# Kernel tuning notes

Measured on AMD Instinct MI355X. Metric: run time of the kernel, lower is better.

The kernel has to match this reference:

```python
import jax, jax.numpy as jnp
import numpy as np
import math

B, N, CS, CZ = 1, 512, 384, 128
GD = 16            # ipa_conf.c_hidden -> num 3D groups G
CH = GD * 3        # per-head hidden = 48
H = 8
PQ, PV = 8, 12
NF = 4             # num_frequencies
INF, EPS = 1e5, 1e-8
CZ4 = CZ // 4


def base_frequencies(num_freqs=NF, base=8.0, max_freq=1.0):
    fs = [min(base ** (-2 * i / num_freqs) * max_freq, max_freq) for i in range(num_freqs)]
    return jnp.asarray(fs, dtype=jnp.float32)


def hat(v):
    # v: [..., 3] -> skew-symmetric [..., 3, 3]
    x, y, z = v[..., 0], v[..., 1], v[..., 2]
    o = jnp.zeros_like(x)
    return jnp.stack([
        jnp.stack([o, -z, y], -1),
        jnp.stack([z, o, -x], -1),
        jnp.stack([-y, x, o], -1)], -2)


def setup_inputs() -> dict:
    key = jax.random.key(0)
    ks = jax.random.split(key, 24)
    std = 0.02
    hc = CH * H
    hpkv = H * (PQ + PV) * 3
    inp = {
        's': jax.random.normal(ks[0], (B, N, CS), jnp.float32),
        'z': jax.random.normal(ks[1], (B, N, N, CZ), jnp.float32),
        'rotvec': jax.random.normal(ks[2], (B, N, 3), jnp.float32),
        'mask': jnp.ones((B, N), jnp.float32),
        'wq': jax.random.normal(ks[3], (CS, hc), jnp.float32) * std,
        'bq': jnp.zeros((hc,), jnp.float32),
        'wkv': jax.random.normal(ks[4], (CS, 2 * hc), jnp.float32) * std,
        'bkv': jnp.zeros((2 * hc,), jnp.float32),
        'wkvp': jax.random.normal(ks[5], (CS, hpkv), jnp.float32) * std,
        'bkvp': jnp.zeros((hpkv,), jnp.float32),
        'wb': jax.random.normal(ks[6], (CZ, H), jnp.float32) * std,
        'bb': jnp.zeros((H,), jnp.float32),
        'wdz': jax.random.normal(ks[7], (CZ, CZ4), jnp.float32) * std,
        'bdz': jnp.zeros((CZ4,), jnp.float32),
        'wout': jax.random.normal(ks[8], (H * (CZ4 + CH + PV * 4), CS), jnp.float32) * std,
        'bout': jnp.zeros((CS,), jnp.float32),
        'log_freq_adj': jax.random.normal(ks[9], (NF,), jnp.float32) * std,
        'group_weights': jax.random.normal(ks[10], (GD,), jnp.float32) * std,
        'freq_weights': jnp.full((NF,), 1.0 / NF, jnp.float32),
    }
    return inp


def reference(s, z, rotvec, mask, wq, bq, wkv, bkv, wkvp, bkvp, wb, bb,
              wdz, bdz, wout, bout, log_freq_adj, group_weights, freq_weights):
    G = GD
    # projections
    q = (s @ wq + bq).reshape(B, N, H, CH)
    kv = (s @ wkv + bkv).reshape(B, N, H, 2 * CH)
    k, v = kv[..., :CH], kv[..., CH:]
    P = PQ + PV
    kvp = (s @ wkvp + bkvp).reshape(B, N, 3, H * P)      # torch split(...,3)+stack(-1)
    kvp = jnp.moveaxis(kvp, -2, -1).reshape(B, N, H, P, 3)
    v_pts = kvp[..., PQ:, :]                             # [B,N,H,PV,3]
    bias = z @ wb + bb                                   # [B,N,N,H]
    # RoPE-inspired multi-frequency Rodrigues rotations
    nrm = jnp.linalg.norm(rotvec, axis=-1, keepdims=True)
    angle = nrm + 1e-8                                   # [B,N,1]
    axis = rotvec / jnp.maximum(nrm, 1e-12)
    freqs = base_frequencies() * jnp.exp(log_freq_adj)   # [F]
    theta = angle * freqs                                # [B,N,F]
    K = hat(axis)                                        # [B,N,3,3]
    K2 = K @ K
    sin_t = jnp.sin(theta)[..., None, None]              # [B,N,F,1,1]
    cos_t = jnp.cos(theta)[..., None, None]
    I3 = jnp.eye(3, dtype=s.dtype)
    R = I3 + sin_t * K[:, :, None] + (1.0 - cos_t) * K2[:, :, None]  # [B,N,F,3,3]
    qg = q.reshape(B, N, H, G, 3)
    kg = k.reshape(B, N, H, G, 3)
    q_rot = jnp.einsum('bnfij,bnhgj->bnhgfi', R, qg)     # [B,N,H,G,F,3]
    k_rot = jnp.einsum('bnfij,bnhgj->bnhgfi', R, kg)
    # aggregation weights (sum over groups, softmax-weighted freqs)
    freq_w = jax.nn.softmax(freq_weights)
    group_w = jax.nn.softplus(group_weights) * math.sqrt(1.0 / G)
    qw = q_rot * freq_w[None, None, None, None, :, None] * group_w[None, None, None, :, None, None]
    scores = jnp.einsum('bihgfc,bjhgfc->bhij', qw, k_rot) / math.sqrt(3.0)
    a = scores + math.sqrt(1.0 / 3.0) * jnp.transpose(bias, (0, 3, 1, 2))
    sq_mask = INF * (mask[:, :, None] * mask[:, None, :] - 1.0)
    a = jax.nn.softmax(a + sq_mask[:, None], axis=-1)    # [B,H,N,N]
    # outputs
    o = jnp.einsum('bhij,bjhc->bihc', a, v).reshape(B, N, H * CH)
    o_pt = jnp.einsum('bhij,bjhpc->bihpc', a, v_pts)     # [B,N,H,PV,3]
    o_pt_norm = jnp.sqrt(jnp.sum(o_pt ** 2, -1) + EPS).reshape(B, N, H * PV)
    o_pt_flat = o_pt.reshape(B, N, H * PV, 3)
    pair_z = z @ wdz + bdz                               # [B,N,N,CZ4]
    o_pair = jnp.einsum('bhij,bijc->bihc', a, pair_z).reshape(B, N, H * CZ4)
    feats = jnp.concatenate([o, o_pt_flat[..., 0], o_pt_flat[..., 1],
                             o_pt_flat[..., 2], o_pt_norm, o_pair], axis=-1)
    return feats @ wout + bout                           # [B,N,CS]
```

## Files before the change

### kernel.cpp

```cpp
#include <hip/hip_runtime.h>
#include <math.h>


#define OFF_PROJ 0
#define SZ_PROJ (512*1632)
#define OFF_QW (OFF_PROJ + SZ_PROJ)
#define SZ_QW (8*512*192)
#define OFF_KST (OFF_QW + SZ_QW)
#define OFF_V (OFF_KST + SZ_QW)
#define SZ_V (512*384)
#define OFF_VP (OFF_V + SZ_V)
#define SZ_VP (512*288)
#define OFF_A (OFF_VP + SZ_VP)
#define SZ_A (8*512*512)
#define OFF_PZ (OFF_A + SZ_A)
#define SZ_PZ (512*512*32)
#define OFF_FEATS (OFF_PZ + SZ_PZ)
#define SZ_FEATS (512*1024)

__global__ __launch_bounds__(256) void proj_kernel(
    const float* __restrict__ s, const float* __restrict__ wq, const float* __restrict__ bq,
    const float* __restrict__ wkv, const float* __restrict__ bkv,
    const float* __restrict__ wkvp, const float* __restrict__ bkvp,
    float* __restrict__ proj)
{
  __shared__ float sA[64][20];
  __shared__ float sB[16][68];
  int ct = blockIdx.x;
  int i0 = blockIdx.y * 64;
  int col0 = ct * 64;
  const float* W; const float* bias; int wld, wcol0;
  if (col0 < 384)       { W = wq;   bias = bq;   wld = 384; wcol0 = col0; }
  else if (col0 < 1152) { W = wkv;  bias = bkv;  wld = 768; wcol0 = col0 - 384; }
  else                  { W = wkvp; bias = bkvp; wld = 480; wcol0 = col0 - 1152; }
  int t = threadIdx.x;
  int tr4 = (t >> 4) * 4;
  int tc4 = (t & 15) * 4;
  float acc[4][4];
  #pragma unroll
  for (int q = 0; q < 4; q++)
    #pragma unroll
    for (int p = 0; p < 4; p++) acc[q][p] = 0.f;
  bool wfull = (wcol0 + 64 <= wld);
  for (int kt = 0; kt < 384; kt += 16){
    {
      int r = t >> 2, k0 = (t & 3) * 4;
      float4 v = *(const float4*)(s + (i0 + r)*384 + kt + k0);
      *(float4*)&sA[r][k0] = v;
    }
    {
      int r = t >> 4, c0 = (t & 15) * 4;
      if (wfull){
        float4 v = *(const float4*)(W + (kt + r)*wld + wcol0 + c0);
        *(float4*)&sB[r][c0] = v;
      } else {
        #pragma unroll
        for (int u = 0; u < 4; u++){
          int wc = wcol0 + c0 + u; if (wc >= wld) wc = wld - 1;
          sB[r][c0+u] = W[(kt + r)*wld + wc];
        }
      }
    }
    __syncthreads();
    #pragma unroll
    for (int k = 0; k < 16; k++){
      float4 bv = *(const float4*)&sB[k][tc4];
      float av[4];
      #pragma unroll
      for (int q = 0; q < 4; q++) av[q] = sA[tr4+q][k];
      #pragma unroll
      for (int q = 0; q < 4; q++){
        acc[q][0] = fmaf(av[q], bv.x, acc[q][0]);
        acc[q][1] = fmaf(av[q], bv.y, acc[q][1]);
        acc[q][2] = fmaf(av[q], bv.z, acc[q][2]);
        acc[q][3] = fmaf(av[q], bv.w, acc[q][3]);
      }
    }
    __syncthreads();
  }
  #pragma unroll
  for (int q = 0; q < 4; q++){
    int row = i0 + tr4 + q;
    #pragma unroll
    for (int p = 0; p < 4; p++){
      int col = col0 + tc4 + p;
      if (col < 1632){
        proj[row*1632 + col] = acc[q][p] + bias[wcol0 + tc4 + p];
      }
    }
  }
}

__global__ __launch_bounds__(128) void node_kernel(
    const float* __restrict__ proj, const float* __restrict__ rotvec,
    const float* __restrict__ lfa, const float* __restrict__ gwts, const float* __restrict__ fwts,
    float* __restrict__ Qw, float* __restrict__ Kst, float* __restrict__ V, float* __restrict__ VP)
{
  int i = blockIdx.x, t = threadIdx.x;
  const float* pr = proj + i*1632;
  float rx = rotvec[i*3], ry = rotvec[i*3+1], rz = rotvec[i*3+2];
  float nrm = sqrtf(rx*rx + ry*ry + rz*rz);
  float angle = nrm + 1e-8f;
  float inv = 1.0f / fmaxf(nrm, 1e-12f);
  float ax = rx*inv, ay = ry*inv, az = rz*inv;
  float f0 = fwts[0], f1 = fwts[1], f2 = fwts[2], f3 = fwts[3];
  float mfw = fmaxf(fmaxf(f0,f1), fmaxf(f2,f3));
  float e0 = expf(f0-mfw), e1 = expf(f1-mfw), e2 = expf(f2-mfw), e3 = expf(f3-mfw);
  float esum = e0+e1+e2+e3;
  float fw[4] = {e0/esum, e1/esum, e2/esum, e3/esum};
  float fq[4] = { 1.0f*expf(lfa[0]), 0.35355339059327373f*expf(lfa[1]),
                  0.125f*expf(lfa[2]), 0.04419417382415922f*expf(lfa[3]) };
  int h = t >> 4, g = t & 15;
  float gw = log1pf(expf(gwts[g])) * 0.25f;
  float q0 = pr[h*48 + g*3 + 0], q1 = pr[h*48 + g*3 + 1], q2 = pr[h*48 + g*3 + 2];
  float k0 = pr[384 + h*96 + g*3 + 0], k1 = pr[384 + h*96 + g*3 + 1], k2 = pr[384 + h*96 + g*3 + 2];
  #pragma unroll
  for (int f = 0; f < 4; f++){
    float th = angle * fq[f];
    float sn = sinf(th), cs = cosf(th), omc = 1.0f - cs;
    float r00 = cs + omc*ax*ax,       r01 = omc*ax*ay - sn*az,  r02 = omc*ax*az + sn*ay;
    float r10 = omc*ay*ax + sn*az,    r11 = cs + omc*ay*ay,     r12 = omc*ay*az - sn*ax;
    float r20 = omc*az*ax - sn*ay,    r21 = omc*az*ay + sn*ax,  r22 = cs + omc*az*az;
    float qr0 = r00*q0 + r01*q1 + r02*q2;
    float qr1 = r10*q0 + r11*q1 + r12*q2;
    float qr2 = r20*q0 + r21*q1 + r22*q2;
    float kr0 = r00*k0 + r01*k1 + r02*k2;
    float kr1 = r10*k0 + r11*k1 + r12*k2;
    float kr2 = r20*k0 + r21*k1 + r22*k2;
    float sc = fw[f] * gw * 0.57735026918962576f;
    int base = (h*512 + i)*192 + (g*4 + f)*3;
    Qw[base+0] = qr0*sc; Qw[base+1] = qr1*sc; Qw[base+2] = qr2*sc;
    Kst[base+0] = kr0;   Kst[base+1] = kr1;   Kst[base+2] = kr2;
  }
  for (int c = t; c < 384; c += 128){
    int hh = c / 48, cc = c % 48;
    V[i*384 + c] = pr[384 + hh*96 + 48 + cc];
  }
  for (int qx = t; qx < 288; qx += 128){
    int ch = qx / 3, c3 = qx % 3;
    int hh = ch / 12, p = ch % 12;
    VP[i*288 + qx] = pr[1152 + c3*160 + hh*20 + 8 + p];
  }
}

__global__ __launch_bounds__(256) void zproj_kernel(
    const float* __restrict__ z, const float* __restrict__ wb, const float* __restrict__ bb,
    const float* __restrict__ wdz, const float* __restrict__ bdz,
    float* __restrict__ biasS, float* __restrict__ PZ)
{
  __shared__ float zs[256][33];
  __shared__ float Wl[40][128];
  int i = blockIdx.y;
  int jt = blockIdx.x;
  int t = threadIdx.x;
  int cg = t >> 6, jg = t & 63;
  for (int e = t; e < 40*128; e += 256){
    int c = e >> 7, k = e & 127;
    Wl[c][k] = (c < 8) ? wb[k*8 + c] : wdz[k*32 + (c - 8)];
  }
  float acc[10][4];
  #pragma unroll
  for (int cc = 0; cc < 10; cc++)
    #pragma unroll
    for (int q = 0; q < 4; q++) acc[cc][q] = 0.f;
  for (int kt = 0; kt < 4; kt++){
    __syncthreads();
    #pragma unroll
    for (int r = 0; r < 8; r++){
      int idx = t + 256*r;
      int jr = idx >> 3, k4 = idx & 7;
      float4 v = *(const float4*)(z + (size_t)(i*512 + jt*256 + jr)*128 + kt*32 + k4*4);
      zs[jr][k4*4+0] = v.x; zs[jr][k4*4+1] = v.y; zs[jr][k4*4+2] = v.z; zs[jr][k4*4+3] = v.w;
    }
    __syncthreads();
    #pragma unroll 4
    for (int k = 0; k < 32; k++){
      float zv[4];
      #pragma unroll
      for (int q = 0; q < 4; q++) zv[q] = zs[q*64 + jg][k];
      #pragma unroll
      for (int cc = 0; cc < 10; cc++){
        float wv = Wl[cg*10 + cc][kt*32 + k];
        #pragma unroll
        for (int q = 0; q < 4; q++) acc[cc][q] = fmaf(zv[q], wv, acc[cc][q]);
      }
    }
  }
  __syncthreads();
  #pragma unroll
  for (int cc = 0; cc < 10; cc++){
    int ch = cg*10 + cc;
    if (ch < 8){
      float bv = bb[ch];
      #pragma unroll
      for (int q = 0; q < 4; q++){
        int j = jt*256 + q*64 + jg;
        biasS[(size_t)ch*262144 + i*512 + j] = 0.57735026918962576f * (acc[cc][q] + bv);
      }
    } else {
      int c = ch - 8;
      float bv = bdz[c];
      #pragma unroll
      for (int q = 0; q < 4; q++){
        zs[q*64 + jg][c] = acc[cc][q] + bv;
      }
    }
  }
  __syncthreads();
  #pragma unroll
  for (int r = 0; r < 8; r++){
    int idx = t + 256*r;
    int jr = idx >> 3, c4 = idx & 7;
    float4 v;
    v.x = zs[jr][c4*4+0]; v.y = zs[jr][c4*4+1]; v.z = zs[jr][c4*4+2]; v.w = zs[jr][c4*4+3];
    *(float4*)(PZ + (size_t)(i*512 + jt*256 + jr)*32 + c4*4) = v;
  }
}

__global__ __launch_bounds__(256) void scores_kernel(
    const float* __restrict__ Qw, const float* __restrict__ Kst,
    const float* __restrict__ mask, float* A)
{
  __shared__ float Qs[16][196];
  __shared__ float Ks[64][196];
  int i0 = blockIdx.x * 16;
  int h = blockIdx.y;
  int t = threadIdx.x;
  int ig = t >> 6, jl = t & 63;
  for (int e = t; e < 16*48; e += 256){
    int r = e / 48, k4 = e % 48;
    float4 v = *(const float4*)(Qw + (size_t)(h*512 + i0 + r)*192 + k4*4);
    *(float4*)&Qs[r][k4*4] = v;
  }
  float lg[4][8];
  for (int jtile = 0; jtile < 8; jtile++){
    __syncthreads();
    for (int e = t; e < 64*48; e += 256){
      int r = e / 48, k4 = e % 48;
      float4 v = *(const float4*)(Kst + (size_t)(h*512 + jtile*64 + r)*192 + k4*4);
      *(float4*)&Ks[r][k4*4] = v;
    }
    __syncthreads();
    float acc[4] = {0.f, 0.f, 0.f, 0.f};
    #pragma unroll 8
    for (int k4 = 0; k4 < 48; k4++){
      float4 kv = *(const float4*)&Ks[jl][k4*4];
      #pragma unroll
      for (int q = 0; q < 4; q++){
        float4 qv = *(const float4*)&Qs[ig*4+q][k4*4];
        acc[q] = fmaf(qv.x, kv.x, acc[q]);
        acc[q] = fmaf(qv.y, kv.y, acc[q]);
        acc[q] = fmaf(qv.z, kv.z, acc[q]);
        acc[q] = fmaf(qv.w, kv.w, acc[q]);
      }
    }
    int j = jtile*64 + jl;
    float mj = mask[j];
    #pragma unroll
    for (int q = 0; q < 4; q++){
      int i = i0 + ig*4 + q;
      float b = A[(size_t)(h*512 + i)*512 + j];
      float mi = mask[i];
      lg[q][jtile] = acc[q] + b + 100000.0f*(mi*mj - 1.0f);
    }
  }
  #pragma unroll
  for (int q = 0; q < 4; q++){
    float m = lg[q][0];
    #pragma unroll
    for (int tl = 1; tl < 8; tl++) m = fmaxf(m, lg[q][tl]);
    for (int off = 32; off > 0; off >>= 1) m = fmaxf(m, __shfl_xor(m, off));
    float ssum = 0.f;
    #pragma unroll
    for (int tl = 0; tl < 8; tl++){ lg[q][tl] = expf(lg[q][tl] - m); ssum += lg[q][tl]; }
    for (int off = 32; off > 0; off >>= 1) ssum += __shfl_xor(ssum, off);
    float invs = 1.0f / ssum;
    int i = i0 + ig*4 + q;
    #pragma unroll
    for (int tl = 0; tl < 8; tl++){
      A[(size_t)(h*512 + i)*512 + tl*64 + jl] = lg[q][tl] * invs;
    }
  }
}

__global__ __launch_bounds__(256) void accum_kernel(
    const float* __restrict__ A, const float* __restrict__ V, const float* __restrict__ VP,
    const float* __restrict__ PZ, float* __restrict__ feats)
{
  __shared__ float a_s[8][64];
  __shared__ float opt_s[288];
  int i = blockIdx.x, t = threadIdx.x;
  int chs[4]; const float* bases[4]; int strides[4]; int hh[4];
  #pragma unroll
  for (int q = 0; q < 4; q++){
    int ch = t + q*256;
    chs[q] = ch;
    if (ch < 384){ hh[q] = ch/48; bases[q] = V + ch; strides[q] = 384; }
    else if (ch < 672){ int qq = ch - 384; hh[q] = qq/36; bases[q] = VP + qq; strides[q] = 288; }
    else if (ch < 928){ int qq = ch - 672; hh[q] = qq/32; bases[q] = PZ + (size_t)i*512*32 + (qq & 31); strides[q] = 32; }
    else { hh[q] = 0; bases[q] = V; strides[q] = 0; }
  }
  float acc[4] = {0.f, 0.f, 0.f, 0.f};
  for (int jtile = 0; jtile < 8; jtile++){
    __syncthreads();
    #pragma unroll
    for (int r = 0; r < 2; r++){
      int e = t + r*256;
      int eh = e >> 6, jj = e & 63;
      a_s[eh][jj] = A[(size_t)(eh*512 + i)*512 + jtile*64 + jj];
    }
    __syncthreads();
    #pragma unroll 4
    for (int jj = 0; jj < 64; jj++){
      int j = jtile*64 + jj;
      #pragma unroll
      for (int q = 0; q < 4; q++){
        acc[q] = fmaf(a_s[hh[q]][jj], bases[q][(size_t)j * strides[q]], acc[q]);
      }
    }
  }
  #pragma unroll
  for (int q = 0; q < 4; q++){
    int ch = chs[q];
    if (ch < 384){ feats[(size_t)i*1024 + ch] = acc[q]; }
    else if (ch < 672){ opt_s[ch - 384] = acc[q]; }
    else if (ch < 928){ feats[(size_t)i*1024 + 768 + (ch - 672)] = acc[q]; }
  }
  __syncthreads();
  if (t < 96){
    float x = opt_s[t*3+0], y = opt_s[t*3+1], zz = opt_s[t*3+2];
    feats[(size_t)i*1024 + 384 + t] = x;
    feats[(size_t)i*1024 + 480 + t] = y;
    feats[(size_t)i*1024 + 576 + t] = zz;
    feats[(size_t)i*1024 + 672 + t] = sqrtf(x*x + y*y + zz*zz + 1e-8f);
  }
}

__global__ __launch_bounds__(256) void out_kernel(
    const float* __restrict__ feats, const float* __restrict__ wout, const float* __restrict__ bout,
    float* __restrict__ out)
{
  __shared__ float sA[32][36];
  __shared__ float sB[32][36];
  int c0 = blockIdx.x * 32;
  int i0 = blockIdx.y * 32;
  int t = threadIdx.x;
  int tr2 = (t >> 4) * 2, tc2 = (t & 15) * 2;
  float a00=0.f, a01=0.f, a10=0.f, a11=0.f;
  for (int kt = 0; kt < 1024; kt += 32){
    {
      int r = t >> 3, k0 = (t & 7) * 4;
      float4 v = *(const float4*)(feats + (size_t)(i0 + r)*1024 + kt + k0);
      *(float4*)&sA[r][k0] = v;
      float4 w = *(const float4*)(wout + (size_t)(kt + r)*384 + c0 + k0);
      *(float4*)&sB[r][k0] = w;
    }
    __syncthreads();
    #pragma unroll
    for (int k = 0; k < 32; k++){
      float b0 = sB[k][tc2], b1 = sB[k][tc2+1];
      float a0 = sA[tr2][k], a1 = sA[tr2+1][k];
      a00 = fmaf(a0,b0,a00); a01 = fmaf(a0,b1,a01);
      a10 = fmaf(a1,b0,a10); a11 = fmaf(a1,b1,a11);
    }
    __syncthreads();
  }
  int c = c0 + tc2, r = i0 + tr2;
  float bo0 = bout[c], bo1 = bout[c+1];
  out[(size_t)r*384 + c]       = a00 + bo0;
  out[(size_t)r*384 + c + 1]   = a01 + bo1;
  out[(size_t)(r+1)*384 + c]   = a10 + bo0;
  out[(size_t)(r+1)*384 + c+1] = a11 + bo1;
}

extern "C" void kernel_launch(void* const* d_in, const int* in_sizes, int n_in,
                              void* d_out, int out_size, void* d_ws, size_t ws_size,
                              hipStream_t stream)
{
  const float* s    = (const float*)d_in[0];
  const float* z    = (const float*)d_in[1];
  const float* rotv = (const float*)d_in[2];
  const float* mask = (const float*)d_in[3];
  const float* wq   = (const float*)d_in[4];
  const float* bq   = (const float*)d_in[5];
  const float* wkv  = (const float*)d_in[6];
  const float* bkv  = (const float*)d_in[7];
  const float* wkvp = (const float*)d_in[8];
  const float* bkvp = (const float*)d_in[9];
  const float* wb   = (const float*)d_in[10];
  const float* bb   = (const float*)d_in[11];
  const float* wdz  = (const float*)d_in[12];
  const float* bdz  = (const float*)d_in[13];
  const float* wout = (const float*)d_in[14];
  const float* bout = (const float*)d_in[15];
  const float* lfa  = (const float*)d_in[16];
  const float* gwts = (const float*)d_in[17];
  const float* fwts = (const float*)d_in[18];
  float* out = (float*)d_out;
  float* ws  = (float*)d_ws;

  float* proj  = ws + OFF_PROJ;
  float* Qw    = ws + OFF_QW;
  float* Kst   = ws + OFF_KST;
  float* V     = ws + OFF_V;
  float* VP    = ws + OFF_VP;
  float* A     = ws + OFF_A;
  float* PZ    = ws + OFF_PZ;
  float* feats = ws + OFF_FEATS;

  proj_kernel  <<<dim3(26, 8),  256, 0, stream>>>(s, wq, bq, wkv, bkv, wkvp, bkvp, proj);
  node_kernel  <<<dim3(512),    128, 0, stream>>>(proj, rotv, lfa, gwts, fwts, Qw, Kst, V, VP);
  zproj_kernel <<<dim3(2, 512), 256, 0, stream>>>(z, wb, bb, wdz, bdz, A, PZ);
  scores_kernel<<<dim3(32, 8),  256, 0, stream>>>(Qw, Kst, mask, A);
  accum_kernel <<<dim3(512),    256, 0, stream>>>(A, V, VP, PZ, feats);
  out_kernel   <<<dim3(12, 16), 256, 0, stream>>>(feats, wout, bout, out);
}
```

Baseline: 450.1 us.

## Reassociate pair projection after attention and retile all GEMM stages

```diff
diff --git a/kernel.cpp b/kernel.cpp
--- a/kernel.cpp
+++ b/kernel.cpp
@@ -13,10 +13,10 @@
 #define SZ_VP (512*288)
 #define OFF_A (OFF_VP + SZ_VP)
 #define SZ_A (8*512*512)
-#define OFF_PZ (OFF_A + SZ_A)
-#define SZ_PZ (512*512*32)
-#define OFF_FEATS (OFF_PZ + SZ_PZ)
+#define OFF_FEATS (OFF_A + SZ_A)
 #define SZ_FEATS (512*1024)
+#define OFF_PART (OFF_FEATS + SZ_FEATS)
+#define SZ_PART (8*512*384)
 
 __global__ __launch_bounds__(256) void proj_kernel(
     const float* __restrict__ s, const float* __restrict__ wq, const float* __restrict__ bq,
@@ -24,69 +24,57 @@
     const float* __restrict__ wkvp, const float* __restrict__ bkvp,
     float* __restrict__ proj)
 {
-  __shared__ float sA[64][20];
-  __shared__ float sB[16][68];
+  __shared__ float sT[384][34];
   int ct = blockIdx.x;
-  int i0 = blockIdx.y * 64;
+  int i0 = blockIdx.y * 32;
   int col0 = ct * 64;
   const float* W; const float* bias; int wld, wcol0;
   if (col0 < 384)       { W = wq;   bias = bq;   wld = 384; wcol0 = col0; }
   else if (col0 < 1152) { W = wkv;  bias = bkv;  wld = 768; wcol0 = col0 - 384; }
   else                  { W = wkvp; bias = bkvp; wld = 480; wcol0 = col0 - 1152; }
   int t = threadIdx.x;
-  int tr4 = (t >> 4) * 4;
-  int tc4 = (t & 15) * 4;
-  float acc[4][4];
-  #pragma unroll
-  for (int q = 0; q < 4; q++)
+  #pragma unroll
+  for (int r = 0; r < 12; r++){
+    int e = t + 256*r;
+    int i = e & 31;
+    int k4 = e >> 5;
+    float4 v = *(const float4*)(s + (size_t)(i0 + i)*384 + k4*4);
+    sT[k4*4+0][i] = v.x; sT[k4*4+1][i] = v.y; sT[k4*4+2][i] = v.z; sT[k4*4+3][i] = v.w;
+  }
+  __syncthreads();
+  int cr = t & 15;
+  int ipair = t >> 4;
+  int ii = ipair * 2;
+  int wc = wcol0 + cr*4;
+  bool valid = (wc + 4 <= wld);
+  int wcc = valid ? wc : (wld - 4);
+  float acc[2][4];
+  #pragma unroll
+  for (int q = 0; q < 2; q++)
     #pragma unroll
     for (int p = 0; p < 4; p++) acc[q][p] = 0.f;
-  bool wfull = (wcol0 + 64 <= wld);
-  for (int kt = 0; kt < 384; kt += 16){
-    {
-      int r = t >> 2, k0 = (t & 3) * 4;
-      float4 v = *(const float4*)(s + (i0 + r)*384 + kt + k0);
-      *(float4*)&sA[r][k0] = v;
-    }
-    {
-      int r = t >> 4, c0 = (t & 15) * 4;
-      if (wfull){
-        float4 v = *(const float4*)(W + (kt + r)*wld + wcol0 + c0);
-        *(float4*)&sB[r][c0] = v;
-      } else {
-        #pragma unroll
-        for (int u = 0; u < 4; u++){
-          int wc = wcol0 + c0 + u; if (wc >= wld) wc = wld - 1;
-          sB[r][c0+u] = W[(kt + r)*wld + wc];
-        }
-      }
-    }
-    __syncthreads();
-    #pragma unroll
-    for (int k = 0; k < 16; k++){
-      float4 bv = *(const float4*)&sB[k][tc4];
-      float av[4];
-      #pragma unroll
-      for (int q = 0; q < 4; q++) av[q] = sA[tr4+q][k];
-      #pragma unroll
-      for (int q = 0; q < 4; q++){
-        acc[q][0] = fmaf(av[q], bv.x, acc[q][0]);
-        acc[q][1] = fmaf(av[q], bv.y, acc[q][1]);
-        acc[q][2] = fmaf(av[q], bv.z, acc[q][2]);
-        acc[q][3] = fmaf(av[q], bv.w, acc[q][3]);
-      }
-    }
-    __syncthreads();
-  }
-  #pragma unroll
-  for (int q = 0; q < 4; q++){
-    int row = i0 + tr4 + q;
-    #pragma unroll
-    for (int p = 0; p < 4; p++){
-      int col = col0 + tc4 + p;
-      if (col < 1632){
-        proj[row*1632 + col] = acc[q][p] + bias[wcol0 + tc4 + p];
-      }
+  #pragma unroll 4
+  for (int k = 0; k < 384; k++){
+    float2 a2 = *(const float2*)&sT[k][ii];
+    float4 w4 = *(const float4*)(W + (size_t)k*wld + wcc);
+    acc[0][0] = fmaf(a2.x, w4.x, acc[0][0]);
+    acc[0][1] = fmaf(a2.x, w4.y, acc[0][1]);
+    acc[0][2] = fmaf(a2.x, w4.z, acc[0][2]);
+    acc[0][3] = fmaf(a2.x, w4.w, acc[0][3]);
+    acc[1][0] = fmaf(a2.y, w4.x, acc[1][0]);
+    acc[1][1] = fmaf(a2.y, w4.y, acc[1][1]);
+    acc[1][2] = fmaf(a2.y, w4.z, acc[1][2]);
+    acc[1][3] = fmaf(a2.y, w4.w, acc[1][3]);
+  }
+  if (valid){
+    float4 bv = *(const float4*)(bias + wc);
+    #pragma unroll
+    for (int q = 0; q < 2; q++){
+      int row = i0 + ii + q;
+      float4 o;
+      o.x = acc[q][0] + bv.x; o.y = acc[q][1] + bv.y;
+      o.z = acc[q][2] + bv.z; o.w = acc[q][3] + bv.w;
+      *(float4*)(proj + (size_t)row*1632 + col0 + cr*4) = o;
     }
   }
 }
@@ -97,7 +85,7 @@
     float* __restrict__ Qw, float* __restrict__ Kst, float* __restrict__ V, float* __restrict__ VP)
 {
   int i = blockIdx.x, t = threadIdx.x;
-  const float* pr = proj + i*1632;
+  const float* pr = proj + (size_t)i*1632;
   float rx = rotvec[i*3], ry = rotvec[i*3+1], rz = rotvec[i*3+2];
   float nrm = sqrtf(rx*rx + ry*ry + rz*rz);
   float angle = nrm + 1e-8f;
@@ -134,86 +122,73 @@
   }
   for (int c = t; c < 384; c += 128){
     int hh = c / 48, cc = c % 48;
-    V[i*384 + c] = pr[384 + hh*96 + 48 + cc];
+    V[(size_t)i*384 + c] = pr[384 + hh*96 + 48 + cc];
   }
   for (int qx = t; qx < 288; qx += 128){
     int ch = qx / 3, c3 = qx % 3;
     int hh = ch / 12, p = ch % 12;
-    VP[i*288 + qx] = pr[1152 + c3*160 + hh*20 + 8 + p];
-  }
-}
-
-__global__ __launch_bounds__(256) void zproj_kernel(
+    VP[(size_t)i*288 + qx] = pr[1152 + c3*160 + hh*20 + 8 + p];
+  }
+}
+
+__global__ __launch_bounds__(256) void zbias_kernel(
     const float* __restrict__ z, const float* __restrict__ wb, const float* __restrict__ bb,
-    const float* __restrict__ wdz, const float* __restrict__ bdz,
-    float* __restrict__ biasS, float* __restrict__ PZ)
-{
-  __shared__ float zs[256][33];
-  __shared__ float Wl[40][128];
+    float* __restrict__ biasS)
+{
+  __shared__ float zs[8*1032];
+  __shared__ float Wl[8*132];
   int i = blockIdx.y;
   int jt = blockIdx.x;
   int t = threadIdx.x;
+  for (int r = 0; r < 4; r++){
+    int e = t + 256*r;
+    int ch = e & 7, k = e >> 3;
+    Wl[ch*132 + k] = wb[k*8 + ch];
+  }
   int cg = t >> 6, jg = t & 63;
-  for (int e = t; e < 40*128; e += 256){
-    int c = e >> 7, k = e & 127;
-    Wl[c][k] = (c < 8) ? wb[k*8 + c] : wdz[k*32 + (c - 8)];
-  }
-  float acc[10][4];
-  #pragma unroll
-  for (int cc = 0; cc < 10; cc++)
-    #pragma unroll
-    for (int q = 0; q < 4; q++) acc[cc][q] = 0.f;
+  int ch0 = cg*2;
+  float acc[2][4];
+  #pragma unroll
+  for (int c = 0; c < 2; c++)
+    #pragma unroll
+    for (int q = 0; q < 4; q++) acc[c][q] = 0.f;
+  const float* zrow = z + ((size_t)i*512 + jt*256)*128;
   for (int kt = 0; kt < 4; kt++){
     __syncthreads();
     #pragma unroll
     for (int r = 0; r < 8; r++){
-      int idx = t + 256*r;
-      int jr = idx >> 3, k4 = idx & 7;
-      float4 v = *(const float4*)(z + (size_t)(i*512 + jt*256 + jr)*128 + kt*32 + k4*4);
-      zs[jr][k4*4+0] = v.x; zs[jr][k4*4+1] = v.y; zs[jr][k4*4+2] = v.z; zs[jr][k4*4+3] = v.w;
-    }
-    __syncthreads();
-    #pragma unroll 4
-    for (int k = 0; k < 32; k++){
-      float zv[4];
-      #pragma unroll
-      for (int q = 0; q < 4; q++) zv[q] = zs[q*64 + jg][k];
-      #pragma unroll
-      for (int cc = 0; cc < 10; cc++){
-        float wv = Wl[cg*10 + cc][kt*32 + k];
-        #pragma unroll
-        for (int q = 0; q < 4; q++) acc[cc][q] = fmaf(zv[q], wv, acc[cc][q]);
-      }
-    }
-  }
-  __syncthreads();
-  #pragma unroll
-  for (int cc = 0; cc < 10; cc++){
-    int ch = cg*10 + cc;
-    if (ch < 8){
-      float bv = bb[ch];
+      int j = (t & 63) + 64*(r & 3);
+      int kq = (t >> 6) + 4*(r >> 2);
+      float4 v = *(const float4*)(zrow + (size_t)j*128 + kt*32 + kq*4);
+      *(float4*)&zs[kq*1032 + j*4] = v;
+    }
+    __syncthreads();
+    const float* wl0 = Wl + ch0*132 + kt*32;
+    const float* wl1 = wl0 + 132;
+    #pragma unroll
+    for (int kq = 0; kq < 8; kq++){
+      float4 w0 = *(const float4*)(wl0 + kq*4);
+      float4 w1 = *(const float4*)(wl1 + kq*4);
       #pragma unroll
       for (int q = 0; q < 4; q++){
-        int j = jt*256 + q*64 + jg;
-        biasS[(size_t)ch*262144 + i*512 + j] = 0.57735026918962576f * (acc[cc][q] + bv);
+        float4 zv = *(const float4*)&zs[kq*1032 + (q*64 + jg)*4];
+        acc[0][q] = fmaf(zv.x, w0.x, acc[0][q]);
+        acc[0][q] = fmaf(zv.y, w0.y, acc[0][q]);
+        acc[0][q] = fmaf(zv.z, w0.z, acc[0][q]);
+        acc[0][q] = fmaf(zv.w, w0.w, acc[0][q]);
+        acc[1][q] = fmaf(zv.x, w1.x, acc[1][q]);
+        acc[1][q] = fmaf(zv.y, w1.y, acc[1][q]);
+        acc[1][q] = fmaf(zv.z, w1.z, acc[1][q]);
+        acc[1][q] = fmaf(zv.w, w1.w, acc[1][q]);
       }
-    } else {
-      int c = ch - 8;
-      float bv = bdz[c];
-      #pragma unroll
-      for (int q = 0; q < 4; q++){
-        zs[q*64 + jg][c] = acc[cc][q] + bv;
-      }
-    }
-  }
-  __syncthreads();
-  #pragma unroll
-  for (int r = 0; r < 8; r++){
-    int idx = t + 256*r;
-    int jr = idx >> 3, c4 = idx & 7;
-    float4 v;
-    v.x = zs[jr][c4*4+0]; v.y = zs[jr][c4*4+1]; v.z = zs[jr][c4*4+2]; v.w = zs[jr][c4*4+3];
-    *(float4*)(PZ + (size_t)(i*512 + jt*256 + jr)*32 + c4*4) = v;
+    }
+  }
+  float b0 = bb[ch0], b1 = bb[ch0+1];
+  #pragma unroll
+  for (int q = 0; q < 4; q++){
+    int j = jt*256 + q*64 + jg;
+    biasS[(size_t)ch0*262144 + i*512 + j]     = 0.57735026918962576f * (acc[0][q] + b0);
+    biasS[(size_t)(ch0+1)*262144 + i*512 + j] = 0.57735026918962576f * (acc[1][q] + b1);
   }
 }
 
@@ -221,156 +196,291 @@
     const float* __restrict__ Qw, const float* __restrict__ Kst,
     const float* __restrict__ mask, float* A)
 {
-  __shared__ float Qs[16][196];
-  __shared__ float Ks[64][196];
+  __shared__ float Ks[4*2056];
+  __shared__ float Qs[4*72];
   int i0 = blockIdx.x * 16;
   int h = blockIdx.y;
   int t = threadIdx.x;
   int ig = t >> 6, jl = t & 63;
-  for (int e = t; e < 16*48; e += 256){
-    int r = e / 48, k4 = e % 48;
-    float4 v = *(const float4*)(Qw + (size_t)(h*512 + i0 + r)*192 + k4*4);
-    *(float4*)&Qs[r][k4*4] = v;
-  }
-  float lg[4][8];
-  for (int jtile = 0; jtile < 8; jtile++){
-    __syncthreads();
-    for (int e = t; e < 64*48; e += 256){
-      int r = e / 48, k4 = e % 48;
-      float4 v = *(const float4*)(Kst + (size_t)(h*512 + jtile*64 + r)*192 + k4*4);
-      *(float4*)&Ks[r][k4*4] = v;
-    }
-    __syncthreads();
-    float acc[4] = {0.f, 0.f, 0.f, 0.f};
-    #pragma unroll 8
-    for (int k4 = 0; k4 < 48; k4++){
-      float4 kv = *(const float4*)&Ks[jl][k4*4];
+  const float* Kb = Kst + (size_t)h*512*192;
+  const float* Qb = Qw + (size_t)(h*512 + i0)*192;
+  float acc[4][8];
+  #pragma unroll
+  for (int q = 0; q < 4; q++)
+    #pragma unroll
+    for (int jt = 0; jt < 8; jt++) acc[q][jt] = 0.f;
+  for (int kc = 0; kc < 12; kc++){
+    __syncthreads();
+    {
+      int k4 = t >> 6;
       #pragma unroll
-      for (int q = 0; q < 4; q++){
-        float4 qv = *(const float4*)&Qs[ig*4+q][k4*4];
-        acc[q] = fmaf(qv.x, kv.x, acc[q]);
-        acc[q] = fmaf(qv.y, kv.y, acc[q]);
-        acc[q] = fmaf(qv.z, kv.z, acc[q]);
-        acc[q] = fmaf(qv.w, kv.w, acc[q]);
+      for (int r = 0; r < 8; r++){
+        int j = (t & 63) + 64*r;
+        float4 v = *(const float4*)(Kb + (size_t)j*192 + kc*16 + k4*4);
+        *(float4*)&Ks[k4*2056 + j*4] = v;
       }
     }
-    int j = jtile*64 + jl;
-    float mj = mask[j];
-    #pragma unroll
-    for (int q = 0; q < 4; q++){
-      int i = i0 + ig*4 + q;
-      float b = A[(size_t)(h*512 + i)*512 + j];
-      float mi = mask[i];
-      lg[q][jtile] = acc[q] + b + 100000.0f*(mi*mj - 1.0f);
-    }
-  }
+    if (t < 64){
+      int qi = t >> 2, k4 = t & 3;
+      float4 v = *(const float4*)(Qb + (size_t)qi*192 + kc*16 + k4*4);
+      *(float4*)&Qs[k4*72 + qi*4] = v;
+    }
+    __syncthreads();
+    #pragma unroll
+    for (int k4 = 0; k4 < 4; k4++){
+      float4 qf[4];
+      #pragma unroll
+      for (int q = 0; q < 4; q++)
+        qf[q] = *(const float4*)&Qs[k4*72 + (ig*4+q)*4];
+      #pragma unroll
+      for (int jt = 0; jt < 8; jt++){
+        float4 kf = *(const float4*)&Ks[k4*2056 + (jt*64 + jl)*4];
+        #pragma unroll
+        for (int q = 0; q < 4; q++){
+          acc[q][jt] = fmaf(qf[q].x, kf.x, acc[q][jt]);
+          acc[q][jt] = fmaf(qf[q].y, kf.y, acc[q][jt]);
+          acc[q][jt] = fmaf(qf[q].z, kf.z, acc[q][jt]);
+          acc[q][jt] = fmaf(qf[q].w, kf.w, acc[q][jt]);
+        }
+      }
+    }
+  }
+  int j0 = jl;
+  float mj[8];
+  #pragma unroll
+  for (int jt = 0; jt < 8; jt++) mj[jt] = mask[jt*64 + j0];
   #pragma unroll
   for (int q = 0; q < 4; q++){
-    float m = lg[q][0];
-    #pragma unroll
-    for (int tl = 1; tl < 8; tl++) m = fmaxf(m, lg[q][tl]);
+    int i = i0 + ig*4 + q;
+    float mi = mask[i];
+    #pragma unroll
+    for (int jt = 0; jt < 8; jt++){
+      float b = A[((size_t)h*512 + i)*512 + jt*64 + j0];
+      acc[q][jt] += b + 100000.0f*(mi*mj[jt] - 1.0f);
+    }
+    float m = acc[q][0];
+    #pragma unroll
+    for (int jt = 1; jt < 8; jt++) m = fmaxf(m, acc[q][jt]);
     for (int off = 32; off > 0; off >>= 1) m = fmaxf(m, __shfl_xor(m, off));
     float ssum = 0.f;
     #pragma unroll
-    for (int tl = 0; tl < 8; tl++){ lg[q][tl] = expf(lg[q][tl] - m); ssum += lg[q][tl]; }
+    for (int jt = 0; jt < 8; jt++){ acc[q][jt] = expf(acc[q][jt] - m); ssum += acc[q][jt]; }
     for (int off = 32; off > 0; off >>= 1) ssum += __shfl_xor(ssum, off);
     float invs = 1.0f / ssum;
-    int i = i0 + ig*4 + q;
-    #pragma unroll
-    for (int tl = 0; tl < 8; tl++){
-      A[(size_t)(h*512 + i)*512 + tl*64 + jl] = lg[q][tl] * invs;
-    }
-  }
-}
-
-__global__ __launch_bounds__(256) void accum_kernel(
+    #pragma unroll
+    for (int jt = 0; jt < 8; jt++){
+      A[((size_t)h*512 + i)*512 + jt*64 + j0] = acc[q][jt] * invs;
+    }
+  }
+}
+
+__global__ __launch_bounds__(256) void paircomb_kernel(
+    const float* __restrict__ A, const float* __restrict__ z,
+    const float* __restrict__ wdz, const float* __restrict__ bdz,
+    float* __restrict__ feats)
+{
+  __shared__ float a_s[2*512*10];
+  __shared__ float Y_s[2*8*132];
+  int i0 = blockIdx.x * 2;
+  int t = threadIdx.x;
+  for (int r = 0; r < 32; r++){
+    int e = t + 256*r;
+    int hh = e >> 10, il = (e >> 9) & 1, j = e & 511;
+    a_s[(il*512 + j)*10 + hh] = A[((size_t)hh*512 + i0 + il)*512 + j];
+  }
+  __syncthreads();
+  int il = t >> 7, u = t & 127, hg = u >> 5, k4 = u & 31;
+  const float* zb = z + ((size_t)(i0 + il)*512)*128 + k4*4;
+  const float* asb = a_s + il*5120 + hg*2;
+  float acc0[4], acc1[4];
+  #pragma unroll
+  for (int m = 0; m < 4; m++){ acc0[m] = 0.f; acc1[m] = 0.f; }
+  #pragma unroll 8
+  for (int j = 0; j < 512; j++){
+    float2 a2 = *(const float2*)&asb[j*10];
+    float4 zv = *(const float4*)(zb + (size_t)j*128);
+    acc0[0] = fmaf(a2.x, zv.x, acc0[0]);
+    acc0[1] = fmaf(a2.x, zv.y, acc0[1]);
+    acc0[2] = fmaf(a2.x, zv.z, acc0[2]);
+    acc0[3] = fmaf(a2.x, zv.w, acc0[3]);
+    acc1[0] = fmaf(a2.y, zv.x, acc1[0]);
+    acc1[1] = fmaf(a2.y, zv.y, acc1[1]);
+    acc1[2] = fmaf(a2.y, zv.z, acc1[2]);
+    acc1[3] = fmaf(a2.y, zv.w, acc1[3]);
+  }
+  float4 y0, y1;
+  y0.x = acc0[0]; y0.y = acc0[1]; y0.z = acc0[2]; y0.w = acc0[3];
+  y1.x = acc1[0]; y1.y = acc1[1]; y1.z = acc1[2]; y1.w = acc1[3];
+  *(float4*)&Y_s[((il*8) + hg*2 + 0)*132 + k4*4] = y0;
+  *(float4*)&Y_s[((il*8) + hg*2 + 1)*132 + k4*4] = y1;
+  __syncthreads();
+  {
+    int il2 = t >> 7, u2 = t & 127, hh = u2 >> 4, cp = u2 & 15;
+    const float* Yr = Y_s + (il2*8 + hh)*132;
+    float s0 = bdz[cp*2], s1 = bdz[cp*2+1];
+    #pragma unroll 8
+    for (int k = 0; k < 128; k++){
+      float yv = Yr[k];
+      float2 w2 = *(const float2*)(wdz + (size_t)k*32 + cp*2);
+      s0 = fmaf(yv, w2.x, s0);
+      s1 = fmaf(yv, w2.y, s1);
+    }
+    float* fp = feats + (size_t)(i0 + il2)*1024 + 768 + hh*32 + cp*2;
+    fp[0] = s0; fp[1] = s1;
+  }
+}
+
+__global__ __launch_bounds__(256) void ovcomb_kernel(
     const float* __restrict__ A, const float* __restrict__ V, const float* __restrict__ VP,
-    const float* __restrict__ PZ, float* __restrict__ feats)
-{
-  __shared__ float a_s[8][64];
-  __shared__ float opt_s[288];
-  int i = blockIdx.x, t = threadIdx.x;
-  int chs[4]; const float* bases[4]; int strides[4]; int hh[4];
+    float* __restrict__ feats)
+{
+  __shared__ float a_s2[8*64*2];
+  __shared__ float opt_s[2][292];
+  int i0 = blockIdx.x * 2;
+  int t = threadIdx.x;
+  bool act = (t < 168);
+  const float* base = V; int stride = 384; int hh = 0;
+  if (act){
+    int ch = t*4;
+    if (ch < 384){ hh = ch/48; base = V + ch; stride = 384; }
+    else { int qq = ch - 384; hh = qq/36; base = VP + qq; stride = 288; }
+  }
+  float acc0[4], acc1[4];
+  #pragma unroll
+  for (int m = 0; m < 4; m++){ acc0[m] = 0.f; acc1[m] = 0.f; }
+  for (int jt = 0; jt < 8; jt++){
+    __syncthreads();
+    #pragma unroll
+    for (int r = 0; r < 4; r++){
+      int e = t + 256*r;
+      int eh = e >> 7, il = (e >> 6) & 1, jj = e & 63;
+      a_s2[(eh*64 + jj)*2 + il] = A[((size_t)eh*512 + i0 + il)*512 + jt*64 + jj];
+    }
+    __syncthreads();
+    if (act){
+      const float* bj = base + (size_t)(jt*64)*stride;
+      #pragma unroll 4
+      for (int jj = 0; jj < 64; jj++){
+        float2 a2 = *(const float2*)&a_s2[(hh*64 + jj)*2];
+        float4 v4 = *(const float4*)(bj + (size_t)jj*stride);
+        acc0[0] = fmaf(a2.x, v4.x, acc0[0]);
+        acc0[1] = fmaf(a2.x, v4.y, acc0[1]);
+        acc0[2] = fmaf(a2.x, v4.z, acc0[2]);
+        acc0[3] = fmaf(a2.x, v4.w, acc0[3]);
+        acc1[0] = fmaf(a2.y, v4.x, acc1[0]);
+        acc1[1] = fmaf(a2.y, v4.y, acc1[1]);
+        acc1[2] = fmaf(a2.y, v4.z, acc1[2]);
+        acc1[3] = fmaf(a2.y, v4.w, acc1[3]);
+      }
+    }
+  }
+  if (act){
+    int ch = t*4;
+    if (ch < 384){
+      float4 o0, o1;
+      o0.x = acc0[0]; o0.y = acc0[1]; o0.z = acc0[2]; o0.w = acc0[3];
+      o1.x = acc1[0]; o1.y = acc1[1]; o1.z = acc1[2]; o1.w = acc1[3];
+      *(float4*)&feats[(size_t)i0*1024 + ch] = o0;
+      *(float4*)&feats[(size_t)(i0+1)*1024 + ch] = o1;
+    } else {
+      int qq = ch - 384;
+      #pragma unroll
+      for (int m = 0; m < 4; m++){
+        opt_s[0][qq + m] = acc0[m];
+        opt_s[1][qq + m] = acc1[m];
+      }
+    }
+  }
+  __syncthreads();
+  if (t < 192){
+    int il = t / 96, p = t % 96;
+    float x = opt_s[il][p*3], y = opt_s[il][p*3+1], zz = opt_s[il][p*3+2];
+    float* fr = feats + (size_t)(i0 + il)*1024;
+    fr[384 + p] = x;
+    fr[480 + p] = y;
+    fr[576 + p] = zz;
+    fr[672 + p] = sqrtf(x*x + y*y + zz*zz + 1e-8f);
+  }
+}
+
+__global__ __launch_bounds__(256) void outgemm_kernel(
+    const float* __restrict__ feats, const float* __restrict__ wout,
+    float* __restrict__ part)
+{
+  __shared__ float fA[32*68];
+  __shared__ float fB[32*68];
+  int ct = blockIdx.x;
+  int it = blockIdx.y;
+  int sk = blockIdx.z;
+  int i0 = it*64, c0 = ct*64, k0 = sk*128;
+  int t = threadIdx.x;
+  int ir = t >> 4, cr = t & 15;
+  float acc[4][4];
+  #pragma unroll
+  for (int q = 0; q < 4; q++)
+    #pragma unroll
+    for (int p = 0; p < 4; p++) acc[q][p] = 0.f;
+  for (int kt = 0; kt < 128; kt += 32){
+    __syncthreads();
+    #pragma unroll
+    for (int r = 0; r < 2; r++){
+      int e = t + 256*r;
+      int i = e & 63, kq = e >> 6;
+      float4 v = *(const float4*)(feats + (size_t)(i0 + i)*1024 + k0 + kt + kq*4);
+      fA[(kq*4+0)*68 + i] = v.x; fA[(kq*4+1)*68 + i] = v.y;
+      fA[(kq*4+2)*68 + i] = v.z; fA[(kq*4+3)*68 + i] = v.w;
+    }
+    #pragma unroll
+    for (int r = 0; r < 2; r++){
+      int e = t + 256*r;
+      int kk = e >> 4, c4 = e & 15;
+      float4 v = *(const float4*)(wout + (size_t)(k0 + kt + kk)*384 + c0 + c4*4);
+      *(float4*)&fB[kk*68 + c4*4] = v;
+    }
+    __syncthreads();
+    #pragma unroll 8
+    for (int k = 0; k < 32; k++){
+      float4 a4 = *(const float4*)&fA[k*68 + ir*4];
+      float4 b4 = *(const float4*)&fB[k*68 + cr*4];
+      acc[0][0] = fmaf(a4.x, b4.x, acc[0][0]);
+      acc[0][1] = fmaf(a4.x, b4.y, acc[0][1]);
+      acc[0][2] = fmaf(a4.x, b4.z, acc[0][2]);
+      acc[0][3] = fmaf(a4.x, b4.w, acc[0][3]);
+      acc[1][0] = fmaf(a4.y, b4.x, acc[1][0]);
+      acc[1][1] = fmaf(a4.y, b4.y, acc[1][1]);
+      acc[1][2] = fmaf(a4.y, b4.z, acc[1][2]);
+      acc[1][3] = fmaf(a4.y, b4.w, acc[1][3]);
+      acc[2][0] = fmaf(a4.z, b4.x, acc[2][0]);
+      acc[2][1] = fmaf(a4.z, b4.y, acc[2][1]);
+      acc[2][2] = fmaf(a4.z, b4.z, acc[2][2]);
+      acc[2][3] = fmaf(a4.z, b4.w, acc[2][3]);
+      acc[3][0] = fmaf(a4.w, b4.x, acc[3][0]);
+      acc[3][1] = fmaf(a4.w, b4.y, acc[3][1]);
+      acc[3][2] = fmaf(a4.w, b4.z, acc[3][2]);
+      acc[3][3] = fmaf(a4.w, b4.w, acc[3][3]);
+    }
+  }
+  float* pb = part + ((size_t)sk*512 + i0)*384 + c0;
   #pragma unroll
   for (int q = 0; q < 4; q++){
-    int ch = t + q*256;
-    chs[q] = ch;
-    if (ch < 384){ hh[q] = ch/48; bases[q] = V + ch; strides[q] = 384; }
-    else if (ch < 672){ int qq = ch - 384; hh[q] = qq/36; bases[q] = VP + qq; strides[q] = 288; }
-    else if (ch < 928){ int qq = ch - 672; hh[q] = qq/32; bases[q] = PZ + (size_t)i*512*32 + (qq & 31); strides[q] = 32; }
-    else { hh[q] = 0; bases[q] = V; strides[q] = 0; }
-  }
-  float acc[4] = {0.f, 0.f, 0.f, 0.f};
-  for (int jtile = 0; jtile < 8; jtile++){
-    __syncthreads();
-    #pragma unroll
-    for (int r = 0; r < 2; r++){
-      int e = t + r*256;
-      int eh = e >> 6, jj = e & 63;
-      a_s[eh][jj] = A[(size_t)(eh*512 + i)*512 + jtile*64 + jj];
-    }
-    __syncthreads();
-    #pragma unroll 4
-    for (int jj = 0; jj < 64; jj++){
-      int j = jtile*64 + jj;
-      #pragma unroll
-      for (int q = 0; q < 4; q++){
-        acc[q] = fmaf(a_s[hh[q]][jj], bases[q][(size_t)j * strides[q]], acc[q]);
-      }
-    }
-  }
-  #pragma unroll
-  for (int q = 0; q < 4; q++){
-    int ch = chs[q];
-    if (ch < 384){ feats[(size_t)i*1024 + ch] = acc[q]; }
-    else if (ch < 672){ opt_s[ch - 384] = acc[q]; }
-    else if (ch < 928){ feats[(size_t)i*1024 + 768 + (ch - 672)] = acc[q]; }
-  }
-  __syncthreads();
-  if (t < 96){
-    float x = opt_s[t*3+0], y = opt_s[t*3+1], zz = opt_s[t*3+2];
-    feats[(size_t)i*1024 + 384 + t] = x;
-    feats[(size_t)i*1024 + 480 + t] = y;
-    feats[(size_t)i*1024 + 576 + t] = zz;
-    feats[(size_t)i*1024 + 672 + t] = sqrtf(x*x + y*y + zz*zz + 1e-8f);
-  }
-}
-
-__global__ __launch_bounds__(256) void out_kernel(
-    const float* __restrict__ feats, const float* __restrict__ wout, const float* __restrict__ bout,
+    float4 o;
+    o.x = acc[q][0]; o.y = acc[q][1]; o.z = acc[q][2]; o.w = acc[q][3];
+    *(float4*)&pb[(size_t)(ir*4 + q)*384 + cr*4] = o;
+  }
+}
+
+__global__ __launch_bounds__(256) void outreduce_kernel(
+    const float* __restrict__ part, const float* __restrict__ bout,
     float* __restrict__ out)
 {
-  __shared__ float sA[32][36];
-  __shared__ float sB[32][36];
-  int c0 = blockIdx.x * 32;
-  int i0 = blockIdx.y * 32;
-  int t = threadIdx.x;
-  int tr2 = (t >> 4) * 2, tc2 = (t & 15) * 2;
-  float a00=0.f, a01=0.f, a10=0.f, a11=0.f;
-  for (int kt = 0; kt < 1024; kt += 32){
-    {
-      int r = t >> 3, k0 = (t & 7) * 4;
-      float4 v = *(const float4*)(feats + (size_t)(i0 + r)*1024 + kt + k0);
-      *(float4*)&sA[r][k0] = v;
-      float4 w = *(const float4*)(wout + (size_t)(kt + r)*384 + c0 + k0);
-      *(float4*)&sB[r][k0] = w;
-    }
-    __syncthreads();
-    #pragma unroll
-    for (int k = 0; k < 32; k++){
-      float b0 = sB[k][tc2], b1 = sB[k][tc2+1];
-      float a0 = sA[tr2][k], a1 = sA[tr2+1][k];
-      a00 = fmaf(a0,b0,a00); a01 = fmaf(a0,b1,a01);
-      a10 = fmaf(a1,b0,a10); a11 = fmaf(a1,b1,a11);
-    }
-    __syncthreads();
-  }
-  int c = c0 + tc2, r = i0 + tr2;
-  float bo0 = bout[c], bo1 = bout[c+1];
-  out[(size_t)r*384 + c]       = a00 + bo0;
-  out[(size_t)r*384 + c + 1]   = a01 + bo1;
-  out[(size_t)(r+1)*384 + c]   = a10 + bo0;
-  out[(size_t)(r+1)*384 + c+1] = a11 + bo1;
+  int e = blockIdx.x*256 + threadIdx.x;
+  float4 acc = *(const float4*)(bout + (e % 96)*4);
+  #pragma unroll
+  for (int sk = 0; sk < 8; sk++){
+    float4 p = *(const float4*)(part + (size_t)sk*196608 + (size_t)e*4);
+    acc.x += p.x; acc.y += p.y; acc.z += p.z; acc.w += p.w;
+  }
+  *(float4*)(out + (size_t)e*4) = acc;
 }
 
 extern "C" void kernel_launch(void* const* d_in, const int* in_sizes, int n_in,
@@ -405,13 +515,15 @@
   float* V     = ws + OFF_V;
   float* VP    = ws + OFF_VP;
   float* A     = ws + OFF_A;
-  float* PZ    = ws + OFF_PZ;
   float* feats = ws + OFF_FEATS;
-
-  proj_kernel  <<<dim3(26, 8),  256, 0, stream>>>(s, wq, bq, wkv, bkv, wkvp, bkvp, proj);
-  node_kernel  <<<dim3(512),    128, 0, stream>>>(proj, rotv, lfa, gwts, fwts, Qw, Kst, V, VP);
-  zproj_kernel <<<dim3(2, 512), 256, 0, stream>>>(z, wb, bb, wdz, bdz, A, PZ);
-  scores_kernel<<<dim3(32, 8),  256, 0, stream>>>(Qw, Kst, mask, A);
-  accum_kernel <<<dim3(512),    256, 0, stream>>>(A, V, VP, PZ, feats);
-  out_kernel   <<<dim3(12, 16), 256, 0, stream>>>(feats, wout, bout, out);
-}
+  float* part  = ws + OFF_PART;
+
+  proj_kernel     <<<dim3(26, 16), 256, 0, stream>>>(s, wq, bq, wkv, bkv, wkvp, bkvp, proj);
+  node_kernel     <<<dim3(512),    128, 0, stream>>>(proj, rotv, lfa, gwts, fwts, Qw, Kst, V, VP);
+  zbias_kernel    <<<dim3(2, 512), 256, 0, stream>>>(z, wb, bb, A);
+  scores_kernel   <<<dim3(32, 8),  256, 0, stream>>>(Qw, Kst, mask, A);
+  paircomb_kernel <<<dim3(256),    256, 0, stream>>>(A, z, wdz, bdz, feats);
+  ovcomb_kernel   <<<dim3(256),    256, 0, stream>>>(A, V, VP, feats);
+  outgemm_kernel  <<<dim3(6, 8, 8),256, 0, stream>>>(feats, wout, part);
+  outreduce_kernel<<<dim3(192),    256, 0, stream>>>(part, bout, out);
+}
```

Result: faster. 422.3 us (-6.2%).
